# Kernel optimization log

Measured on AMD Instinct MI355X. Metric: run time of the kernel, lower is better.

## Reference

```python
import jax, jax.numpy as jnp
import numpy as np

HEADS = 16
LN_EPS = 1e-5

def setup_inputs() -> dict:
    key = jax.random.key(0)
    ks = jax.random.split(key, 8)
    B, S, NT = 4, 1024, 1024
    sc = 1.0 / np.sqrt(NT)
    return {
        "x": jax.random.normal(ks[0], (B, S, NT), dtype=jnp.float32),
        "Wq": jax.random.normal(ks[1], (NT, NT), dtype=jnp.float32) * sc,
        "bq": jax.random.normal(ks[2], (NT,), dtype=jnp.float32) * 0.02,
        "Wk": jax.random.normal(ks[3], (NT, NT), dtype=jnp.float32) * sc,
        "bk": jax.random.normal(ks[4], (NT,), dtype=jnp.float32) * 0.02,
        "Wv": jax.random.normal(ks[5], (NT, NT), dtype=jnp.float32) * sc,
        "bv": jax.random.normal(ks[6], (NT,), dtype=jnp.float32) * 0.02,
        "gamma": jnp.ones((NT,), dtype=jnp.float32),
        "beta": jnp.zeros((NT,), dtype=jnp.float32),
    }

def reference(x, Wq, bq, Wk, bk, Wv, bv, gamma, beta):
    B, S, nt = x.shape
    heads = HEADS
    dph = nt // heads
    # torch nn.Linear: y = x @ W.T + b
    q = x @ Wq.T + bq
    k = x @ Wk.T + bk
    v = x @ Wv.T + bv
    # torch .view(B*heads, -1, dph) is a row-major reshape (interleaved split)
    q = q.reshape(B * heads, -1, dph)
    k = k.reshape(B * heads, -1, dph)
    v = v.reshape(B * heads, -1, dph)
    # scaled scores; scale uses last dim of the score matrix (== seq len here)
    att = jnp.einsum('bid,bjd->bij', q, k)
    scale = att.shape[-1] ** (-0.5)
    att = jax.nn.softmax(jax.nn.relu(att * scale), axis=-1)
    # dropout in eval mode -> identity
    at_sum_sum = att.sum(axis=1).reshape(B, heads, -1)  # [B, heads, S]
    context = jnp.einsum('bij,bjd->bid', att, v).reshape(B, -1, nt)
    h = x + context
    mu = h.mean(axis=-1, keepdims=True)
    var = h.var(axis=-1, keepdims=True)
    out = (h - mu) * jax.lax.rsqrt(var + LN_EPS) * gamma + beta
    return out, at_sum_sum
```

## Files before the change

kernel.cpp:

```cpp
#include <hip/hip_runtime.h>
#include <hip/hip_bf16.h>
#include <cstdint>
#include <cstddef>


typedef short short8 __attribute__((ext_vector_type(8)));
typedef short short4v __attribute__((ext_vector_type(4)));
typedef float f32x4 __attribute__((ext_vector_type(4)));

#define MFMA32(a, b, c) __builtin_amdgcn_mfma_f32_16x16x32_bf16(a, b, c, 0, 0, 0)
#define MFMA16x16(a, b, c) __builtin_amdgcn_mfma_f32_16x16x16bf16_1k(a, b, c, 0, 0, 0)
#define QSCALE 0.045084220027780106f

__device__ __forceinline__ short f2bf(float f) {
  union { float f; uint32_t u; } x; x.f = f;
  uint32_t u = x.u + 0x7fffu + ((x.u >> 16) & 1u);
  return (short)(u >> 16);
}

__device__ __forceinline__ uint32_t pk_bf16_trunc(float lo, float hi) {
  return __builtin_amdgcn_perm(__float_as_uint(hi), __float_as_uint(lo),
                               0x07060302u);
}

#define GLDS16(gp, lp)                                                        \
  __builtin_amdgcn_global_load_lds(                                           \
      (const __attribute__((address_space(1))) void*)(gp),                    \
      (__attribute__((address_space(3))) void*)(lp), 16, 0, 0)

__global__ __launch_bounds__(256) void convert_kernel(
    const float* __restrict__ x, const float* __restrict__ wq,
    const float* __restrict__ wk, const float* __restrict__ wv,
    short* __restrict__ xb, short* __restrict__ wb,
    float* __restrict__ out2) {
  if (blockIdx.x >= 7168) {
    const int idx = (blockIdx.x - 7168) * 256 + threadIdx.x;
    *(f32x4*)(out2 + (size_t)idx * 4) = (f32x4){0.f, 0.f, 0.f, 0.f};
    return;
  }
  const long XN = 4L * 1024 * 1024, WN = 1024L * 1024;
  long e = (long)(blockIdx.x * blockDim.x + threadIdx.x) * 4;
  const float* src; short* dst;
  if (e < XN)               { src = x  + e;                dst = xb + e; }
  else if (e < XN + WN)     { src = wq + (e - XN);         dst = wb + (e - XN); }
  else if (e < XN + 2 * WN) { src = wk + (e - XN - WN);    dst = wb + (e - XN); }
  else                      { src = wv + (e - XN - 2*WN);  dst = wb + (e - XN); }
  f32x4 v = *(const f32x4*)src;
  short4v o;
  o[0] = f2bf(v[0]); o[1] = f2bf(v[1]); o[2] = f2bf(v[2]); o[3] = f2bf(v[3]);
  *(short4v*)dst = o;
}

__global__ __launch_bounds__(256, 3) void qkv_gemm(
    const short* __restrict__ xb, const short* __restrict__ wb,
    const float* __restrict__ bq, const float* __restrict__ bk,
    const float* __restrict__ bv, short* __restrict__ qb,
    short* __restrict__ kb, short* __restrict__ vtp) {
  __shared__ short As[128 * 64];
  __shared__ short Bs[128 * 64];
  const int tid = threadIdx.x;
  const int lane = tid & 63;
  const int lm = lane & 15, quad = lane >> 4;
  const int wave = tid >> 6, wy = wave >> 1, wx = wave & 1;
  const int f = blockIdx.x + (blockIdx.y << 3);
  const int r8 = f & 7, s = f >> 3;
  const int m0 = (((r8 >> 1) << 3) + (s & 7)) * 128;
  const int n0 = (((r8 & 1) << 2) + (s >> 3)) * 128;
  const int z = blockIdx.z;
  const short* w = wb + (size_t)z * (1024 * 1024);
  const float* bias = (z == 0) ? bq : (z == 1) ? bk : bv;
  const float scl = (z == 0) ? QSCALE : 1.0f;

  const int srow = tid >> 3;
  const int schk = (tid & 7) ^ (srow & 7);
  const short* gA = xb + (size_t)(m0 + srow) * 1024 + schk * 8;
  const short* gB = w  + (size_t)(n0 + srow) * 1024 + schk * 8;
  short* lA = As + tid * 8;
  short* lB = Bs + tid * 8;

  f32x4 acc[4][4];
#pragma unroll
  for (int i = 0; i < 4; i++)
#pragma unroll
    for (int j = 0; j < 4; j++) acc[i][j] = (f32x4){0.f, 0.f, 0.f, 0.f};

  for (int k0 = 0; k0 < 1024; k0 += 64) {
#pragma unroll
    for (int q = 0; q < 4; q++) {
      GLDS16(gA + k0 + q * 32 * 1024, lA + q * 2048);
      GLDS16(gB + k0 + q * 32 * 1024, lB + q * 2048);
    }
    __syncthreads();
#pragma unroll
    for (int ks = 0; ks < 2; ks++) {
      const int ck = (((ks << 2) + quad) ^ (lm & 7)) * 8;
      short8 a[4], b[4];
#pragma unroll
      for (int t = 0; t < 4; t++) {
        a[t] = *(const short8*)(As + (wy * 64 + t * 16 + lm) * 64 + ck);
        b[t] = *(const short8*)(Bs + (wx * 64 + t * 16 + lm) * 64 + ck);
      }
#pragma unroll
      for (int mt = 0; mt < 4; mt++)
#pragma unroll
        for (int nt = 0; nt < 4; nt++)
          acc[mt][nt] = MFMA32(a[mt], b[nt], acc[mt][nt]);
    }
    __syncthreads();
  }
  if (z == 2) {
#pragma unroll
    for (int nt = 0; nt < 4; nt++) {
      const int n = n0 + wx * 64 + nt * 16 + lm;
      const float bn = bias[n];
      const size_t nbase = (size_t)((n >> 4) & 3) * 16384 +
                           (size_t)((((n >> 8) & 3) * 16 + (n & 15)) * 4 +
                                    ((n >> 6) & 3));
#pragma unroll
      for (int mt = 0; mt < 4; mt++) {
#pragma unroll
        for (int r = 0; r < 4; r++) {
          const int m = m0 + wy * 64 + mt * 16 + quad * 4 + r;
          vtp[(size_t)(m >> 6) * 65536 + nbase + (size_t)(m & 63) * 256] =
              f2bf(acc[mt][nt][r] + bn);
        }
      }
    }
  } else {
    short* out = (z == 0) ? qb : kb;
#pragma unroll
    for (int nt = 0; nt < 4; nt++) {
      const int n = n0 + wx * 64 + nt * 16 + lm;
      const float bn = bias[n];
#pragma unroll
      for (int mt = 0; mt < 4; mt++) {
        const int mb = m0 + wy * 64 + mt * 16 + quad * 4;
#pragma unroll
        for (int r = 0; r < 4; r++)
          out[(size_t)(mb + r) * 1024 + n] = f2bf((acc[mt][nt][r] + bn) * scl);
      }
    }
  }
}

__global__ __launch_bounds__(256, 2) void attn_kernel(
    const short* __restrict__ qb, const short* __restrict__ kb,
    const short* __restrict__ vtp, const float* __restrict__ x,
    const float* __restrict__ gamma, const float* __restrict__ beta,
    float* __restrict__ out1, float* __restrict__ out2) {
  __shared__ short Ks[3][64 * 64];
  __shared__ short Vs[3][4 * 4 * 256];

  const int tid = threadIdx.x;
  const int lane = tid & 63, wave = tid >> 6;
  const int lm = lane & 15, quad = lane >> 4;
  const int bid = blockIdx.x;
  const int h = ((bid >> 6) << 3) + (bid & 7);
  const int bb = (bid >> 3) & 7;
  const short* Qh = qb + (size_t)h * 65536;
  const short* Kh = kb + (size_t)h * 65536;
  const short* Vp = vtp + (size_t)h * 65536;
  const int i0 = bb * 128 + wave * 32;

  const short8 qA0 = *(const short8*)(Qh + (size_t)(i0 + lm) * 64 + quad * 8);
  const short8 qA1 = *(const short8*)(Qh + (size_t)(i0 + lm) * 64 + 32 + quad * 8);
  const short8 qB0 = *(const short8*)(Qh + (size_t)(i0 + 16 + lm) * 64 + quad * 8);
  const short8 qB1 = *(const short8*)(Qh + (size_t)(i0 + 16 + lm) * 64 + 32 + quad * 8);

  const int c0 = tid, c1 = tid + 256;
  const short* gK0 = Kh + (size_t)(c0 >> 3) * 64 + ((c0 & 7) ^ ((c0 >> 3) & 7)) * 8;
  const short* gK1 = Kh + (size_t)(c1 >> 3) * 64 + ((c1 & 7) ^ ((c1 >> 3) & 7)) * 8;
  const short* gV0 = Vp + (c0 >> 7) * 16384 + ((c0 >> 5) & 3) * 256 + (c0 & 31) * 8;
  const short* gV1 = Vp + (c1 >> 7) * 16384 + ((c1 >> 5) & 3) * 256 + (c1 & 31) * 8;
  const int lK0 = c0 * 8, lK1 = c1 * 8;

#define ATTN_STAGE(c, buf)                                                    \
  do {                                                                        \
    const int ko_ = ((c) & 15) * 4096, vo_ = ((c) & 15) * 1024;               \
    GLDS16(gK0 + ko_, &Ks[buf][0] + lK0);                                     \
    GLDS16(gK1 + ko_, &Ks[buf][0] + lK1);                                     \
    GLDS16(gV0 + vo_, &Vs[buf][0] + lK0);                                     \
    GLDS16(gV1 + vo_, &Vs[buf][0] + lK1);                                     \
  } while (0)

#define ATTN_STAGE2(c, buf)                                                   \
  do {                                                                        \
    const int ko_ = ((c) & 15) * 4096;                                        \
    GLDS16(gK0 + ko_, &Ks[buf][0] + lK0);                                     \
    GLDS16(gK1 + ko_, &Ks[buf][0] + lK1);                                     \
  } while (0)

  f32x4 accA[4], accB[4];
#pragma unroll
  for (int t = 0; t < 4; t++) {
    accA[t] = (f32x4){0.f, 0.f, 0.f, 0.f};
    accB[t] = (f32x4){0.f, 0.f, 0.f, 0.f};
  }
  float dsA[4] = {0.f, 0.f, 0.f, 0.f};
  float dsB[4] = {0.f, 0.f, 0.f, 0.f};

  const int swz0 = (quad ^ (lm & 7)) * 8;
  const int swz1 = ((quad + 4) ^ (lm & 7)) * 8;

  ATTN_STAGE(0, 0);
  ATTN_STAGE(1, 1);

  for (int ch = 0; ch < 16; ch++) {
    const int b = ch % 3, bs = (ch + 2) % 3;
    asm volatile("s_waitcnt vmcnt(4)" ::: "memory");
    __builtin_amdgcn_s_barrier();
    if (ch < 15) ATTN_STAGE(ch + 2, bs);
    __builtin_amdgcn_s_setprio(1);
#pragma unroll
    for (int jj = 0; jj < 4; jj++) {
      const short* krow = &Ks[b][(jj * 16 + lm) * 64];
      const short8 kf0 = *(const short8*)(krow + swz0);
      const short8 kf1 = *(const short8*)(krow + swz1);
      f32x4 zA = {0.f, 0.f, 0.f, 0.f};
      zA = MFMA32(kf0, qA0, zA);
      zA = MFMA32(kf1, qA1, zA);
      f32x4 zB = {0.f, 0.f, 0.f, 0.f};
      zB = MFMA32(kf0, qB0, zB);
      zB = MFMA32(kf1, qB1, zB);
      float pA[4], pB[4];
#pragma unroll
      for (int r = 0; r < 4; r++) {
        pA[r] = __builtin_amdgcn_exp2f(fmaxf(zA[r], 0.f));
        dsA[r] += pA[r];
        pB[r] = __builtin_amdgcn_exp2f(fmaxf(zB[r], 0.f));
        dsB[r] += pB[r];
      }
      union { uint32_t u[2]; short4v s; } puA, puB;
      puA.u[0] = pk_bf16_trunc(pA[0], pA[1]);
      puA.u[1] = pk_bf16_trunc(pA[2], pA[3]);
      puB.u[0] = pk_bf16_trunc(pB[0], pB[1]);
      puB.u[1] = pk_bf16_trunc(pB[2], pB[3]);
      const short* vbase = &Vs[b][jj * 256 + lane * 4];
#pragma unroll
      for (int dt = 0; dt < 4; dt++) {
        const short4v vtf = *(const short4v*)(vbase + dt * 1024);
        accA[dt] = MFMA16x16(vtf, puA.s, accA[dt]);
        accB[dt] = MFMA16x16(vtf, puB.s, accB[dt]);
      }
    }
    __builtin_amdgcn_s_setprio(0);
  }
  asm volatile("s_waitcnt vmcnt(0)" ::: "memory");

  float tA = (dsA[0] + dsA[1]) + (dsA[2] + dsA[3]);
  tA += __shfl_xor(tA, 16);
  tA += __shfl_xor(tA, 32);
  float tB = (dsB[0] + dsB[1]) + (dsB[2] + dsB[3]);
  tB += __shfl_xor(tB, 16);
  tB += __shfl_xor(tB, 32);
  const float rvA = 1.f / tA;
  const float rvB = 1.f / tB;

  float rvsA[4], rvsB[4];
#pragma unroll
  for (int r = 0; r < 4; r++) {
    rvsA[r] = __shfl(rvA, quad * 4 + r);
    rvsB[r] = __shfl(rvB, quad * 4 + r);
  }
  __syncthreads();
  float* cs = (float*)&Vs[0][0];

  ATTN_STAGE2(0, 0);
  ATTN_STAGE2(1, 1);

  for (int ch = 0; ch < 16; ch++) {
    const int b = ch % 3, bs = (ch + 2) % 3;
    asm volatile("s_waitcnt vmcnt(2)" ::: "memory");
    __builtin_amdgcn_s_barrier();
    if (ch < 15) ATTN_STAGE2(ch + 2, bs);
    __builtin_amdgcn_s_setprio(1);
#pragma unroll
    for (int jj = 0; jj < 4; jj++) {
      const short* krow = &Ks[b][(jj * 16 + lm) * 64];
      const short8 kf0 = *(const short8*)(krow + swz0);
      const short8 kf1 = *(const short8*)(krow + swz1);
      f32x4 zA = {0.f, 0.f, 0.f, 0.f};
      zA = MFMA32(qA0, kf0, zA);
      zA = MFMA32(qA1, kf1, zA);
      f32x4 zB = {0.f, 0.f, 0.f, 0.f};
      zB = MFMA32(qB0, kf0, zB);
      zB = MFMA32(qB1, kf1, zB);
      float v = 0.f;
#pragma unroll
      for (int r = 0; r < 4; r++) {
        v += __builtin_amdgcn_exp2f(fmaxf(zA[r], 0.f)) * rvsA[r]
           + __builtin_amdgcn_exp2f(fmaxf(zB[r], 0.f)) * rvsB[r];
      }
      v += __shfl_xor(v, 16);
      v += __shfl_xor(v, 32);
      if (quad == 0)
        cs[wave * 1024 + ch * 64 + jj * 16 + lm] = v;
    }
    __builtin_amdgcn_s_setprio(0);
  }
  asm volatile("s_waitcnt vmcnt(0)" ::: "memory");
  __syncthreads();
#pragma unroll
  for (int s = 0; s < 4; s++) {
    const int j = s * 256 + tid;
    const float t4 = (cs[j] + cs[1024 + j]) + (cs[2048 + j] + cs[3072 + j]);
    atomicAdd(out2 + h * 1024 + j, t4);
  }

  const int mA = h * 64 + bb * 8 + wave * 2;
  const int nb = lm * 64 + quad * 4;
#pragma unroll
  for (int tile = 0; tile < 2; tile++) {
    const int m = mA + tile;
    const f32x4* accT = tile ? accB : accA;
    const float rv = tile ? rvB : rvA;
    const float* xr = x + (size_t)m * 1024;
    float hv[4][4], s1 = 0.f, s2 = 0.f;
#pragma unroll
    for (int dt = 0; dt < 4; dt++) {
      f32x4 xv = *(const f32x4*)(xr + nb + dt * 16);
#pragma unroll
      for (int r = 0; r < 4; r++) {
        const float v = xv[r] + accT[dt][r] * rv;
        hv[dt][r] = v; s1 += v; s2 += v * v;
      }
    }
#pragma unroll
    for (int mk = 1; mk < 64; mk <<= 1) {
      s1 += __shfl_xor(s1, mk);
      s2 += __shfl_xor(s2, mk);
    }
    const float mu = s1 * (1.f / 1024.f);
    const float var = s2 * (1.f / 1024.f) - mu * mu;
    const float rstd = rsqrtf(var + 1e-5f);
    float* orow = out1 + (size_t)m * 1024;
#pragma unroll
    for (int dt = 0; dt < 4; dt++) {
      f32x4 gv = *(const f32x4*)(gamma + nb + dt * 16);
      f32x4 bv2 = *(const f32x4*)(beta + nb + dt * 16);
      f32x4 ov;
#pragma unroll
      for (int r = 0; r < 4; r++)
        ov[r] = (hv[dt][r] - mu) * rstd * gv[r] + bv2[r];
      *(f32x4*)(orow + nb + dt * 16) = ov;
    }
  }
}

extern "C" void kernel_launch(void* const* d_in, const int* in_sizes, int n_in,
                              void* d_out, int out_size, void* d_ws, size_t ws_size,
                              hipStream_t stream) {
  const float* x  = (const float*)d_in[0];
  const float* Wq = (const float*)d_in[1];
  const float* bq = (const float*)d_in[2];
  const float* Wk = (const float*)d_in[3];
  const float* bk = (const float*)d_in[4];
  const float* Wv = (const float*)d_in[5];
  const float* bv = (const float*)d_in[6];
  const float* gamma = (const float*)d_in[7];
  const float* beta  = (const float*)d_in[8];

  float* out1 = (float*)d_out;
  float* out2 = out1 + 4L * 1024 * 1024;

  short* xb = (short*)d_ws;
  short* wb = xb + 4L * 1024 * 1024;
  short* qb = wb + 3L * 1024 * 1024;
  short* kb = qb + 4L * 1024 * 1024;
  short* vtp = kb + 4L * 1024 * 1024;

  convert_kernel<<<7232, 256, 0, stream>>>(x, Wq, Wk, Wv, xb, wb, out2);
  qkv_gemm<<<dim3(8, 32, 3), 256, 0, stream>>>(xb, wb, bq, bk, bv, qb, kb, vtp);
  attn_kernel<<<512, 256, 0, stream>>>(qb, kb, vtp, x, gamma, beta, out1, out2);
}
```

Baseline: 164.4 us.

## Rewrite QKV GEMM as 256x256 tile, 8-wave kernel with multi-stage LDS pipeline

The QKV projection GEMM moves from 128x128 tiles with 4 waves and a single LDS buffer to 256x256 tiles with 8 waves. A prefetch pipeline loads A tiles two k-steps ahead into six LDS slots and double-buffers B. The inner loop is split into four phases, each issuing a global-to-LDS stage, then a barrier, then MFMAs at raised priority, so loads overlap compute and each LDS tile is reused more. The cost is 192 blocks (fewer than the CU count, so one wave of blocks), heavier register and LDS use, and a more fragile barrier and waitcnt schedule.

Measured after the change: 179.8 us. 1.09x slower.

```diff
diff --git a/kernel.cpp b/kernel.cpp
--- a/kernel.cpp
+++ b/kernel.cpp
@@ -51,21 +51,20 @@
   *(short4v*)dst = o;
 }
 
-__global__ __launch_bounds__(256, 3) void qkv_gemm(
+__global__ __launch_bounds__(512, 1) void qkv_gemm8(
     const short* __restrict__ xb, const short* __restrict__ wb,
     const float* __restrict__ bq, const float* __restrict__ bk,
     const float* __restrict__ bv, short* __restrict__ qb,
     short* __restrict__ kb, short* __restrict__ vtp) {
-  __shared__ short As[128 * 64];
-  __shared__ short Bs[128 * 64];
+  __shared__ short As[6][8192];
+  __shared__ short Bs[2][8192];
+
   const int tid = threadIdx.x;
   const int lane = tid & 63;
   const int lm = lane & 15, quad = lane >> 4;
-  const int wave = tid >> 6, wy = wave >> 1, wx = wave & 1;
-  const int f = blockIdx.x + (blockIdx.y << 3);
-  const int r8 = f & 7, s = f >> 3;
-  const int m0 = (((r8 >> 1) << 3) + (s & 7)) * 128;
-  const int n0 = (((r8 & 1) << 2) + (s >> 3)) * 128;
+  const int wid = tid >> 6;
+  const int wr = wid >> 2, wc = wid & 3;
+  const int m0 = blockIdx.y * 256, n0 = blockIdx.x * 256;
   const int z = blockIdx.z;
   const short* w = wb + (size_t)z * (1024 * 1024);
   const float* bias = (z == 0) ? bq : (z == 1) ? bk : bv;
@@ -75,52 +74,101 @@
   const int schk = (tid & 7) ^ (srow & 7);
   const short* gA = xb + (size_t)(m0 + srow) * 1024 + schk * 8;
   const short* gB = w  + (size_t)(n0 + srow) * 1024 + schk * 8;
-  short* lA = As + tid * 8;
-  short* lB = Bs + tid * 8;
-
-  f32x4 acc[4][4];
-#pragma unroll
-  for (int i = 0; i < 4; i++)
+
+#define STAGE_A(kt, h, slot)                                                  \
+  do {                                                                        \
+    const short* s0_ = gA + (size_t)((h) * 128) * 1024 + (kt) * 64;           \
+    GLDS16(s0_, &As[slot][0] + tid * 8);                                      \
+    GLDS16(s0_ + 64 * 1024, &As[slot][0] + 4096 + tid * 8);                   \
+  } while (0)
+#define STAGE_B(kt, h)                                                        \
+  do {                                                                        \
+    const short* s0_ = gB + (size_t)((h) * 128) * 1024 + (kt) * 64;           \
+    GLDS16(s0_, &Bs[h][0] + tid * 8);                                         \
+    GLDS16(s0_ + 64 * 1024, &Bs[h][0] + 4096 + tid * 8);                      \
+  } while (0)
+
+  f32x4 acc[8][4];
+#pragma unroll
+  for (int i = 0; i < 8; i++)
 #pragma unroll
     for (int j = 0; j < 4; j++) acc[i][j] = (f32x4){0.f, 0.f, 0.f, 0.f};
 
-  for (int k0 = 0; k0 < 1024; k0 += 64) {
-#pragma unroll
-    for (int q = 0; q < 4; q++) {
-      GLDS16(gA + k0 + q * 32 * 1024, lA + q * 2048);
-      GLDS16(gB + k0 + q * 32 * 1024, lB + q * 2048);
-    }
-    __syncthreads();
-#pragma unroll
-    for (int ks = 0; ks < 2; ks++) {
-      const int ck = (((ks << 2) + quad) ^ (lm & 7)) * 8;
-      short8 a[4], b[4];
-#pragma unroll
-      for (int t = 0; t < 4; t++) {
-        a[t] = *(const short8*)(As + (wy * 64 + t * 16 + lm) * 64 + ck);
-        b[t] = *(const short8*)(Bs + (wx * 64 + t * 16 + lm) * 64 + ck);
-      }
-#pragma unroll
-      for (int mt = 0; mt < 4; mt++)
-#pragma unroll
-        for (int nt = 0; nt < 4; nt++)
-          acc[mt][nt] = MFMA32(a[mt], b[nt], acc[mt][nt]);
-    }
-    __syncthreads();
-  }
+  const int swz0 = (quad ^ (lm & 7)) * 8;
+  const int swz1 = ((quad + 4) ^ (lm & 7)) * 8;
+
+  STAGE_A(0, 0, 0);
+  STAGE_A(0, 1, 1);
+  STAGE_B(0, 0);
+  STAGE_B(0, 1);
+  STAGE_A(1, 0, 2);
+  STAGE_A(1, 1, 3);
+  asm volatile("s_waitcnt vmcnt(4)" ::: "memory");
+  __builtin_amdgcn_sched_barrier(0);
+  __builtin_amdgcn_s_barrier();
+
+  int rdslot = wr;
+  int st0 = 4, st1 = 5;
+
+  short8 bfr[4][2], afr[2][2];
+
+#define QPHASE(P, STG, TAIL)                                                  \
+  do {                                                                        \
+    afr[0][0] = *(const short8*)(Ah + ((P * 2 + 0) * 16 + lm) * 64 + swz0);   \
+    afr[0][1] = *(const short8*)(Ah + ((P * 2 + 0) * 16 + lm) * 64 + swz1);   \
+    afr[1][0] = *(const short8*)(Ah + ((P * 2 + 1) * 16 + lm) * 64 + swz0);   \
+    afr[1][1] = *(const short8*)(Ah + ((P * 2 + 1) * 16 + lm) * 64 + swz1);   \
+    STG;                                                                      \
+    __builtin_amdgcn_s_barrier();                                             \
+    __builtin_amdgcn_s_setprio(1);                                            \
+    _Pragma("unroll")                                                         \
+    for (int am = 0; am < 2; am++)                                            \
+      _Pragma("unroll")                                                       \
+      for (int nt = 0; nt < 4; nt++)                                          \
+        _Pragma("unroll")                                                     \
+        for (int kk = 0; kk < 2; kk++)                                        \
+          acc[P * 2 + am][nt] =                                               \
+              MFMA32(afr[am][kk], bfr[nt][kk], acc[P * 2 + am][nt]);          \
+    __builtin_amdgcn_s_setprio(0);                                            \
+    TAIL;                                                                     \
+    __builtin_amdgcn_s_barrier();                                             \
+  } while (0)
+
+#pragma unroll 1
+  for (int U = 0; U < 16; ++U) {
+    const int ktn1 = (U + 1) & 15, ktn2 = (U + 2) & 15;
+    const short* Ah = &As[rdslot][0];
+#pragma unroll
+    for (int nt = 0; nt < 4; nt++) {
+      const int rb = ((wc & 1) * 64 + nt * 16 + lm) * 64;
+      bfr[nt][0] = *(const short8*)(&Bs[wc >> 1][0] + rb + swz0);
+      bfr[nt][1] = *(const short8*)(&Bs[wc >> 1][0] + rb + swz1);
+    }
+    QPHASE(0, STAGE_A(ktn2, 0, st0), );
+    QPHASE(1, STAGE_B(ktn1, 0), );
+    QPHASE(2, STAGE_B(ktn1, 1), );
+    QPHASE(3, STAGE_A(ktn2, 1, st1),
+           asm volatile("s_waitcnt vmcnt(2)" ::: "memory");
+           __builtin_amdgcn_sched_barrier(0));
+    rdslot += 2; if (rdslot >= 6) rdslot -= 6;
+    st0 += 2;    if (st0 >= 6)    st0 -= 6;
+    st1 += 2;    if (st1 >= 6)    st1 -= 6;
+  }
+  asm volatile("s_waitcnt vmcnt(0)" ::: "memory");
+
   if (z == 2) {
 #pragma unroll
     for (int nt = 0; nt < 4; nt++) {
-      const int n = n0 + wx * 64 + nt * 16 + lm;
+      const int n = n0 + wc * 64 + nt * 16 + lm;
       const float bn = bias[n];
       const size_t nbase = (size_t)((n >> 4) & 3) * 16384 +
                            (size_t)((((n >> 8) & 3) * 16 + (n & 15)) * 4 +
                                     ((n >> 6) & 3));
 #pragma unroll
-      for (int mt = 0; mt < 4; mt++) {
+      for (int mt = 0; mt < 8; mt++) {
 #pragma unroll
         for (int r = 0; r < 4; r++) {
-          const int m = m0 + wy * 64 + mt * 16 + quad * 4 + r;
+          const int m = m0 + wr * 128 + mt * 16 + quad * 4 + r;
           vtp[(size_t)(m >> 6) * 65536 + nbase + (size_t)(m & 63) * 256] =
               f2bf(acc[mt][nt][r] + bn);
         }
@@ -130,11 +178,11 @@
     short* out = (z == 0) ? qb : kb;
 #pragma unroll
     for (int nt = 0; nt < 4; nt++) {
-      const int n = n0 + wx * 64 + nt * 16 + lm;
+      const int n = n0 + wc * 64 + nt * 16 + lm;
       const float bn = bias[n];
 #pragma unroll
-      for (int mt = 0; mt < 4; mt++) {
-        const int mb = m0 + wy * 64 + mt * 16 + quad * 4;
+      for (int mt = 0; mt < 8; mt++) {
+        const int mb = m0 + wr * 128 + mt * 16 + quad * 4;
 #pragma unroll
         for (int r = 0; r < 4; r++)
           out[(size_t)(mb + r) * 1024 + n] = f2bf((acc[mt][nt][r] + bn) * scl);
@@ -370,6 +418,6 @@
   short* vtp = kb + 4L * 1024 * 1024;
 
   convert_kernel<<<7232, 256, 0, stream>>>(x, Wq, Wk, Wv, xb, wb, out2);
-  qkv_gemm<<<dim3(8, 32, 3), 256, 0, stream>>>(xb, wb, bq, bk, bv, qb, kb, vtp);
+  qkv_gemm8<<<dim3(4, 16, 3), 512, 0, stream>>>(xb, wb, bq, bk, bv, qb, kb, vtp);
   attn_kernel<<<512, 256, 0, stream>>>(qb, kb, vtp, x, gamma, beta, out1, out2);
 }
```
